# Performance work log

Measured on AMD Instinct MI355X. Metric: run time of the kernel, lower is better.

## Reference

```python
import jax, jax.numpy as jnp
import numpy as np

B, M = 64, 2048
D_LLM = 4096
D_T, D_P, D_C = 256, 512, 1024
NH_T, NH_P, NH_C = 4, 8, 16
S_T, S_P, S_C = 4, 8, 4
LN_EPS = 1e-5


def setup_inputs() -> dict:
    key = jax.random.key(0)
    ks = iter(jax.random.split(key, 48))
    def n(shape, s=0.02):
        return jax.random.normal(next(ks), shape, jnp.float32) * s
    inp = {
        "hidden_state": jax.random.normal(next(ks), (B, D_LLM), jnp.float32),
        "time_fiber": jax.random.normal(next(ks), (M, D_T), jnp.float32),
        "topic_fiber": jax.random.normal(next(ks), (M, D_P), jnp.float32),
        "ctx_fiber": jax.random.normal(next(ks), (M, D_C), jnp.float32),
        "mem_mask": jnp.zeros((B, M), bool),
        # BundleQueryHeads: Linear(d_LLM -> d_F_*) per bundle (torch weight layout (out,in))
        "Wq_time": n((D_T, D_LLM)), "bq_time": jnp.zeros((D_T,), jnp.float32),
        "Wq_topic": n((D_P, D_LLM)), "bq_topic": jnp.zeros((D_P,), jnp.float32),
        "Wq_ctx": n((D_C, D_LLM)), "bq_ctx": jnp.zeros((D_C,), jnp.float32),
        # nn.MultiheadAttention packed in_proj (3d, d) and out_proj (d, d)
        "Wqkv_time": n((3 * D_T, D_T)), "bqkv_time": jnp.zeros((3 * D_T,), jnp.float32),
        "Wo_time": n((D_T, D_T)), "bo_time": jnp.zeros((D_T,), jnp.float32),
        "Wqkv_topic": n((3 * D_P, D_P)), "bqkv_topic": jnp.zeros((3 * D_P,), jnp.float32),
        "Wo_topic": n((D_P, D_P)), "bo_topic": jnp.zeros((D_P,), jnp.float32),
        "Wqkv_ctx": n((3 * D_C, D_C)), "bqkv_ctx": jnp.zeros((3 * D_C,), jnp.float32),
        "Wo_ctx": n((D_C, D_C)), "bo_ctx": jnp.zeros((D_C,), jnp.float32),
        # per-slot lifts stacked: (slots, d_F, d_LLM) for einsum 'bd,sde->bse'
        "Wlift_time": n((S_T, D_T, D_LLM)), "blift_time": jnp.zeros((S_T, D_LLM), jnp.float32),
        "Wlift_topic": n((S_P, D_P, D_LLM)), "blift_topic": jnp.zeros((S_P, D_LLM), jnp.float32),
        "Wlift_ctx": n((S_C, D_C, D_LLM)), "blift_ctx": jnp.zeros((S_C, D_LLM), jnp.float32),
        "ln_g": jnp.ones((D_LLM,), jnp.float32),
        "ln_b": jnp.zeros((D_LLM,), jnp.float32),
    }
    return inp


def _mha1(q, kv, Wqkv, bqkv, Wo, bo, nh, mask):
    """Single-query-token MHA. q: (B,d); kv: (M,d) shared across batch; mask: (B,M) True=ignore."""
    d = q.shape[-1]
    hd = d // nh
    Wq, Wk, Wv = jnp.split(Wqkv, 3, axis=0)
    bq, bk, bv = jnp.split(bqkv, 3, axis=0)
    qp = (q @ Wq.T + bq).reshape(-1, nh, hd)    # (B,h,hd)
    kp = (kv @ Wk.T + bk).reshape(-1, nh, hd)   # (M,h,hd)
    vp = (kv @ Wv.T + bv).reshape(-1, nh, hd)   # (M,h,hd)
    scale = 1.0 / np.float32(np.sqrt(hd))
    scores = jnp.einsum('bhd,mhd->bhm', qp, kp) * scale  # (B,h,M)
    scores = jnp.where(mask[:, None, :], jnp.float32(-1e9), scores)
    attn = jax.nn.softmax(scores, axis=-1)
    out = jnp.einsum('bhm,mhd->bhd', attn, vp).reshape(-1, d)  # (B,d)
    return out @ Wo.T + bo


def _layernorm(x, g, b):
    mu = jnp.mean(x, axis=-1, keepdims=True)
    var = jnp.mean((x - mu) ** 2, axis=-1, keepdims=True)
    return (x - mu) * jax.lax.rsqrt(var + LN_EPS) * g + b


def reference(hidden_state, time_fiber, topic_fiber, ctx_fiber, mem_mask,
              Wq_time, bq_time, Wq_topic, bq_topic, Wq_ctx, bq_ctx,
              Wqkv_time, bqkv_time, Wo_time, bo_time,
              Wqkv_topic, bqkv_topic, Wo_topic, bo_topic,
              Wqkv_ctx, bqkv_ctx, Wo_ctx, bo_ctx,
              Wlift_time, blift_time, Wlift_topic, blift_topic, Wlift_ctx, blift_ctx,
              ln_g, ln_b):
    # bundle query heads
    q_time = hidden_state @ Wq_time.T + bq_time
    q_topic = hidden_state @ Wq_topic.T + bq_topic
    q_ctx = hidden_state @ Wq_ctx.T + bq_ctx
    # three single-token cross attentions
    o_time = _mha1(q_time, time_fiber, Wqkv_time, bqkv_time, Wo_time, bo_time, NH_T, mem_mask)
    o_topic = _mha1(q_topic, topic_fiber, Wqkv_topic, bqkv_topic, Wo_topic, bo_topic, NH_P, mem_mask)
    o_ctx = _mha1(q_ctx, ctx_fiber, Wqkv_ctx, bqkv_ctx, Wo_ctx, bo_ctx, NH_C, mem_mask)
    # per-slot lifts, batched across slots
    slots_time = jnp.einsum('bd,sde->bse', o_time, Wlift_time) + blift_time[None]
    slots_topic = jnp.einsum('bd,sde->bse', o_topic, Wlift_topic) + blift_topic[None]
    slots_ctx = jnp.einsum('bd,sde->bse', o_ctx, Wlift_ctx) + blift_ctx[None]
    prefix = jnp.concatenate([slots_time, slots_topic, slots_ctx], axis=1)  # (B, L_mem, d_LLM)
    return _layernorm(prefix, ln_g, ln_b)
```

## Files before the change

kernel.cpp:

```cpp
#include <hip/hip_runtime.h>
#include <cstdint>
#include <cstddef>

typedef __attribute__((ext_vector_type(8))) short short8;
typedef __attribute__((ext_vector_type(4))) float floatx4;

__device__ __forceinline__ unsigned short f2bf(float f) {
    unsigned int u = __builtin_bit_cast(unsigned int, f);
    u += 0x7fffu + ((u >> 16) & 1u);
    return (unsigned short)(u >> 16);
}
__device__ __forceinline__ float bflo(unsigned int u) {
    return __builtin_bit_cast(float, u << 16);
}
__device__ __forceinline__ short8 pack8(float4 a, float4 b) {
    short8 r;
    r[0] = (short)f2bf(a.x); r[1] = (short)f2bf(a.y);
    r[2] = (short)f2bf(a.z); r[3] = (short)f2bf(a.w);
    r[4] = (short)f2bf(b.x); r[5] = (short)f2bf(b.y);
    r[6] = (short)f2bf(b.z); r[7] = (short)f2bf(b.w);
    return r;
}

struct SubGemm {
    const float* A; const float* W; const float* bias;
    float* Cf; unsigned short* Ch;
    int K, N, Kc, nj, ni, nkz, mode, ldc;
};
struct GemmBatch { SubGemm d[16]; int start[16]; int nd; };

__global__ __launch_bounds__(256) void gemm_batch(GemmBatch gb)
{
    __shared__ short As[64 * 40];
    __shared__ __align__(16) char Braw[32 * 132 * 4];
    short* Bs  = (short*)Braw;
    float* Bsf = (float*)Braw;

    const int bx = blockIdx.x;
    int di = 0;
#pragma unroll 1
    for (int i = 1; i < gb.nd; ++i) if (bx >= gb.start[i]) di = i;
    const SubGemm g = gb.d[di];
    int local = bx - gb.start[di];
    const int jb = local % g.nj; local /= g.nj;
    const int ib = local % g.ni;
    const int kz = local / g.ni;

    const int tid = threadIdx.x;
    const int w = tid >> 6, lane = tid & 63;
    const int quad = lane >> 4, l16 = lane & 15;
    const int noff = w * 32;

    const int rA = tid >> 2, cA = (tid & 3) * 8;
    const float* pa = g.A + (size_t)(ib * 64 + rA) * g.K + kz * g.Kc + cA;

    floatx4 acc[4][2] = {};

    if (g.mode <= 1) {
        const int rB = tid >> 1, cB = (tid & 1) * 16;
        const float* pb = g.W + (size_t)(jb * 128 + rB) * g.K + kz * g.Kc + cB;
        float4 a0 = *(const float4*)(pa), a1 = *(const float4*)(pa + 4);
        float4 b0 = *(const float4*)(pb),     b1 = *(const float4*)(pb + 4);
        float4 b2 = *(const float4*)(pb + 8), b3 = *(const float4*)(pb + 12);
#pragma unroll 1
        for (int k0 = 0; k0 < g.Kc; k0 += 32) {
            *(short8*)&As[rA * 40 + cA]     = pack8(a0, a1);
            *(short8*)&Bs[rB * 40 + cB]     = pack8(b0, b1);
            *(short8*)&Bs[rB * 40 + cB + 8] = pack8(b2, b3);
            __syncthreads();
            if (k0 + 32 < g.Kc) {
                pa += 32; pb += 32;
                a0 = *(const float4*)(pa);     a1 = *(const float4*)(pa + 4);
                b0 = *(const float4*)(pb);     b1 = *(const float4*)(pb + 4);
                b2 = *(const float4*)(pb + 8); b3 = *(const float4*)(pb + 12);
            }
            short8 af[4], bfr[2];
#pragma unroll
            for (int r = 0; r < 4; ++r)
                af[r] = *(const short8*)&As[(r * 16 + l16) * 40 + quad * 8];
#pragma unroll
            for (int c = 0; c < 2; ++c)
                bfr[c] = *(const short8*)&Bs[(noff + c * 16 + l16) * 40 + quad * 8];
#pragma unroll
            for (int r = 0; r < 4; ++r)
#pragma unroll
                for (int c = 0; c < 2; ++c)
                    acc[r][c] = __builtin_amdgcn_mfma_f32_16x16x32_bf16(af[r], bfr[c], acc[r][c], 0, 0, 0);
            __syncthreads();
        }
    } else {
        const int rK = tid >> 3, cN = (tid & 7) * 16;
        const float* pb = g.W + (size_t)rK * g.N + jb * 128 + cN;
        float4 a0 = *(const float4*)(pa), a1 = *(const float4*)(pa + 4);
        float4 b0 = *(const float4*)(pb),     b1 = *(const float4*)(pb + 4);
        float4 b2 = *(const float4*)(pb + 8), b3 = *(const float4*)(pb + 12);
#pragma unroll 1
        for (int k0 = 0; k0 < g.Kc; k0 += 32) {
            *(short8*)&As[rA * 40 + cA] = pack8(a0, a1);
            *(float4*)&Bsf[rK * 132 + cN]      = b0;
            *(float4*)&Bsf[rK * 132 + cN + 4]  = b1;
            *(float4*)&Bsf[rK * 132 + cN + 8]  = b2;
            *(float4*)&Bsf[rK * 132 + cN + 12] = b3;
            __syncthreads();
            if (k0 + 32 < g.Kc) {
                pa += 32; pb += (size_t)32 * g.N;
                a0 = *(const float4*)(pa);     a1 = *(const float4*)(pa + 4);
                b0 = *(const float4*)(pb);     b1 = *(const float4*)(pb + 4);
                b2 = *(const float4*)(pb + 8); b3 = *(const float4*)(pb + 12);
            }
            short8 af[4], bfr[2];
#pragma unroll
            for (int r = 0; r < 4; ++r)
                af[r] = *(const short8*)&As[(r * 16 + l16) * 40 + quad * 8];
#pragma unroll
            for (int c = 0; c < 2; ++c) {
                const int colb = noff + c * 16 + l16;
#pragma unroll
                for (int i = 0; i < 8; ++i)
                    bfr[c][i] = (short)f2bf(Bsf[(quad * 8 + i) * 132 + colb]);
            }
#pragma unroll
            for (int r = 0; r < 4; ++r)
#pragma unroll
                for (int c = 0; c < 2; ++c)
                    acc[r][c] = __builtin_amdgcn_mfma_f32_16x16x32_bf16(af[r], bfr[c], acc[r][c], 0, 0, 0);
            __syncthreads();
        }
    }

#pragma unroll
    for (int r = 0; r < 4; ++r)
#pragma unroll
        for (int c = 0; c < 2; ++c) {
            const int col = jb * 128 + noff + c * 16 + l16;
            const float bj = (g.mode == 1 && kz != 0) ? 0.f : g.bias[col];
#pragma unroll
            for (int q = 0; q < 4; ++q) {
                const int row = ib * 64 + r * 16 + quad * 4 + q;
                const float v = acc[r][c][q] + bj;
                if (g.mode == 0)
                    g.Ch[(size_t)row * g.ldc + col] = f2bf(v);
                else if (g.mode == 1) {
                    if (g.nkz > 1) atomicAdd(&g.Cf[(size_t)row * g.ldc + col], v);
                    else           g.Cf[(size_t)row * g.ldc + col] = v;
                } else
                    g.Cf[(size_t)row * g.ldc + col] = v;
            }
        }
}

__global__ __launch_bounds__(256) void qk_batch(
    const float* __restrict__ qp_t, const float* __restrict__ qp_p, const float* __restrict__ qp_c,
    const unsigned short* __restrict__ kv_t, const unsigned short* __restrict__ kv_p, const unsigned short* __restrict__ kv_c,
    float* __restrict__ S_t, float* __restrict__ S_p, float* __restrict__ S_c)
{
    __shared__ short As[64 * 72];
    __shared__ short Bs[128 * 72];
    const int hy = blockIdx.y;
    const float* qp; const unsigned short* kv; float* S; int d, h;
    if (hy < 4)       { qp = qp_t; kv = kv_t; S = S_t; d = 256;  h = hy; }
    else if (hy < 12) { qp = qp_p; kv = kv_p; S = S_p; d = 512;  h = hy - 4; }
    else              { qp = qp_c; kv = kv_c; S = S_c; d = 1024; h = hy - 12; }

    const int j0 = blockIdx.x * 128;
    const int tid = threadIdx.x;
    const int w = tid >> 6, lane = tid & 63;
    const int quad = lane >> 4, l16 = lane & 15;
    const int noff = w * 32;
    const int twoD = 2 * d;

    {
        const int b = tid >> 2, kc = (tid & 3) * 16;
        const float* ga = qp + (size_t)b * d + h * 64 + kc;
        float4 a0 = *(const float4*)(ga + 0), a1 = *(const float4*)(ga + 4);
        float4 a2 = *(const float4*)(ga + 8), a3 = *(const float4*)(ga + 12);
        *(short8*)&As[b * 72 + kc + 0] = pack8(a0, a1);
        *(short8*)&As[b * 72 + kc + 8] = pack8(a2, a3);
    }
    {
        const int m = tid >> 1, hf = (tid & 1) * 32;
        const unsigned short* gb = kv + (size_t)(j0 + m) * twoD + h * 64 + hf;
        uint4 b0 = *(const uint4*)(gb + 0),  b1 = *(const uint4*)(gb + 8);
        uint4 b2 = *(const uint4*)(gb + 16), b3 = *(const uint4*)(gb + 24);
        *(uint4*)&Bs[m * 72 + hf + 0]  = b0;
        *(uint4*)&Bs[m * 72 + hf + 8]  = b1;
        *(uint4*)&Bs[m * 72 + hf + 16] = b2;
        *(uint4*)&Bs[m * 72 + hf + 24] = b3;
    }
    __syncthreads();

    floatx4 acc[4][2] = {};
#pragma unroll
    for (int k0 = 0; k0 < 64; k0 += 32) {
        short8 af[4], bfr[2];
#pragma unroll
        for (int r = 0; r < 4; ++r)
            af[r] = *(const short8*)&As[(r * 16 + l16) * 72 + k0 + quad * 8];
#pragma unroll
        for (int c = 0; c < 2; ++c)
            bfr[c] = *(const short8*)&Bs[(noff + c * 16 + l16) * 72 + k0 + quad * 8];
#pragma unroll
        for (int r = 0; r < 4; ++r)
#pragma unroll
            for (int c = 0; c < 2; ++c)
                acc[r][c] = __builtin_amdgcn_mfma_f32_16x16x32_bf16(af[r], bfr[c], acc[r][c], 0, 0, 0);
    }
#pragma unroll
    for (int r = 0; r < 4; ++r)
#pragma unroll
        for (int c = 0; c < 2; ++c) {
            int col = j0 + noff + c * 16 + l16;
#pragma unroll
            for (int q = 0; q < 4; ++q) {
                int row = r * 16 + quad * 4 + q;
                S[((size_t)h * 64 + row) * 2048 + col] = acc[r][c][q] * 0.125f;
            }
        }
}

__global__ __launch_bounds__(256) void softmax_pv_batch(
    const float* __restrict__ S_t, const float* __restrict__ S_p, const float* __restrict__ S_c,
    const unsigned short* __restrict__ kv_t, const unsigned short* __restrict__ kv_p, const unsigned short* __restrict__ kv_c,
    const uint8_t* __restrict__ mask,
    float* __restrict__ o_t, float* __restrict__ o_p, float* __restrict__ o_c)
{
    const int hy = blockIdx.x, b = blockIdx.y;
    const float* S; const unsigned short* kv; float* o; int d, h;
    if (hy < 4)       { S = S_t; kv = kv_t; o = o_t; d = 256;  h = hy; }
    else if (hy < 12) { S = S_p; kv = kv_p; o = o_p; d = 512;  h = hy - 4; }
    else              { S = S_c; kv = kv_c; o = o_c; d = 1024; h = hy - 12; }

    const int tid = threadIdx.x;
    __shared__ __align__(16) float sc[2048];
    __shared__ float red[4];
    __shared__ float part[4][64];
    __shared__ float s_max, s_sum;

    const float* Sr = S + ((size_t)h * 64 + b) * 2048;
    const uint8_t* mr = mask + (size_t)b * 2048;

    float lmax = -1e30f;
    for (int m = tid; m < 2048; m += 256) {
        float s = Sr[m];
        if (mr[m]) s = -1e9f;
        sc[m] = s;
        lmax = fmaxf(lmax, s);
    }
#pragma unroll
    for (int off = 32; off; off >>= 1) lmax = fmaxf(lmax, __shfl_down(lmax, off));
    if ((tid & 63) == 0) red[tid >> 6] = lmax;
    __syncthreads();
    if (tid == 0) s_max = fmaxf(fmaxf(red[0], red[1]), fmaxf(red[2], red[3]));
    __syncthreads();
    const float mx = s_max;

    float lsum = 0.f;
    for (int m = tid; m < 2048; m += 256) {
        float e = __expf(sc[m] - mx);
        sc[m] = e;
        lsum += e;
    }
#pragma unroll
    for (int off = 32; off; off >>= 1) lsum += __shfl_down(lsum, off);
    if ((tid & 63) == 0) red[tid >> 6] = lsum;
    __syncthreads();
    if (tid == 0) s_sum = red[0] + red[1] + red[2] + red[3];
    __syncthreads();

    const int lane = tid & 63, w = tid >> 6;
    const int twoD = 2 * d;
    const unsigned short* vcol = kv + d + h * 64 + lane;
    float acc = 0.f;
    const int m0 = w * 512;
#pragma unroll 1
    for (int m = m0; m < m0 + 512; m += 8) {
#pragma unroll
        for (int j = 0; j < 8; ++j)
            acc += sc[m + j] * bflo((unsigned int)vcol[(size_t)(m + j) * twoD]);
    }
    part[w][lane] = acc;
    __syncthreads();
    if (tid < 64) {
        float r = (part[0][tid] + part[1][tid] + part[2][tid] + part[3][tid]) / s_sum;
        o[(size_t)b * d + h * 64 + tid] = r;
    }
}

__global__ __launch_bounds__(256) void ln_kernel(
    float* __restrict__ x, const float* __restrict__ g, const float* __restrict__ bb)
{
    const int row = blockIdx.x;
    float* xr = x + (size_t)row * 4096;
    const int tid = threadIdx.x;
    float v[16];
    float sum = 0.f, sumsq = 0.f;
#pragma unroll
    for (int i = 0; i < 16; ++i) {
        v[i] = xr[tid + i * 256];
        sum += v[i];
        sumsq += v[i] * v[i];
    }
    __shared__ float rs[4], rq[4];
#pragma unroll
    for (int off = 32; off; off >>= 1) {
        sum += __shfl_down(sum, off);
        sumsq += __shfl_down(sumsq, off);
    }
    if ((tid & 63) == 0) { rs[tid >> 6] = sum; rq[tid >> 6] = sumsq; }
    __syncthreads();
    const float ts = rs[0] + rs[1] + rs[2] + rs[3];
    const float tq = rq[0] + rq[1] + rq[2] + rq[3];
    const float mu = ts * (1.f / 4096.f);
    const float var = tq * (1.f / 4096.f) - mu * mu;
    const float r = rsqrtf(var + 1e-5f);
#pragma unroll
    for (int i = 0; i < 16; ++i) {
        int e = tid + i * 256;
        xr[e] = (v[i] - mu) * r * g[e] + bb[e];
    }
}

static void addg(GemmBatch& G, int& tot,
                 const float* A, const float* W, const float* bias,
                 float* Cf, unsigned short* Ch,
                 int K, int N, int Kc, int nj, int ni, int nkz, int mode, int ldc)
{
    SubGemm& s = G.d[G.nd];
    s.A = A; s.W = W; s.bias = bias; s.Cf = Cf; s.Ch = Ch;
    s.K = K; s.N = N; s.Kc = Kc; s.nj = nj; s.ni = ni; s.nkz = nkz;
    s.mode = mode; s.ldc = ldc;
    G.start[G.nd] = tot;
    tot += nj * ni * nkz;
    G.nd++;
}

extern "C" void kernel_launch(void* const* d_in, const int* in_sizes, int n_in,
                              void* d_out, int out_size, void* d_ws, size_t ws_size,
                              hipStream_t stream)
{
    const float*   hs     = (const float*)d_in[0];
    const float*   fib_t  = (const float*)d_in[1];
    const float*   fib_p  = (const float*)d_in[2];
    const float*   fib_c  = (const float*)d_in[3];
    const uint8_t* mask   = (const uint8_t*)d_in[4];
    const float* Wq_t   = (const float*)d_in[5];  const float* bq_t   = (const float*)d_in[6];
    const float* Wq_p   = (const float*)d_in[7];  const float* bq_p   = (const float*)d_in[8];
    const float* Wq_c   = (const float*)d_in[9];  const float* bq_c   = (const float*)d_in[10];
    const float* Wqkv_t = (const float*)d_in[11]; const float* bqkv_t = (const float*)d_in[12];
    const float* Wo_t   = (const float*)d_in[13]; const float* bo_t   = (const float*)d_in[14];
    const float* Wqkv_p = (const float*)d_in[15]; const float* bqkv_p = (const float*)d_in[16];
    const float* Wo_p   = (const float*)d_in[17]; const float* bo_p   = (const float*)d_in[18];
    const float* Wqkv_c = (const float*)d_in[19]; const float* bqkv_c = (const float*)d_in[20];
    const float* Wo_c   = (const float*)d_in[21]; const float* bo_c   = (const float*)d_in[22];
    const float* Wl_t   = (const float*)d_in[23]; const float* bl_t   = (const float*)d_in[24];
    const float* Wl_p   = (const float*)d_in[25]; const float* bl_p   = (const float*)d_in[26];
    const float* Wl_c   = (const float*)d_in[27]; const float* bl_c   = (const float*)d_in[28];
    const float* ln_g   = (const float*)d_in[29]; const float* ln_b   = (const float*)d_in[30];

    char* wsb = (char*)d_ws;
    float* q_t  = (float*)wsb; wsb += 64 * 256 * 4;
    float* q_p  = (float*)wsb; wsb += 64 * 512 * 4;
    float* q_c  = (float*)wsb; wsb += 64 * 1024 * 4;
    float* qp_t = (float*)wsb; wsb += 64 * 256 * 4;
    float* qp_p = (float*)wsb; wsb += 64 * 512 * 4;
    float* qp_c = (float*)wsb; wsb += 64 * 1024 * 4;
    float* po_t = (float*)wsb; wsb += 64 * 256 * 4;
    float* po_p = (float*)wsb; wsb += 64 * 512 * 4;
    float* po_c = (float*)wsb; wsb += 64 * 1024 * 4;
    size_t zbytes = (size_t)(wsb - (char*)d_ws);
    float* o_t  = (float*)wsb; wsb += 64 * 256 * 4;
    float* o_p  = (float*)wsb; wsb += 64 * 512 * 4;
    float* o_c  = (float*)wsb; wsb += 64 * 1024 * 4;
    unsigned short* kv_t = (unsigned short*)wsb; wsb += 2048 * 512 * 2;
    unsigned short* kv_p = (unsigned short*)wsb; wsb += 2048 * 1024 * 2;
    unsigned short* kv_c = (unsigned short*)wsb; wsb += 2048 * 2048 * 2;
    float* S_t = (float*)wsb; wsb += (size_t)4  * 64 * 2048 * 4;
    float* S_p = (float*)wsb; wsb += (size_t)8  * 64 * 2048 * 4;
    float* S_c = (float*)wsb; wsb += (size_t)16 * 64 * 2048 * 4;
    float* out = (float*)d_out;

    const dim3 blk(256);
    hipMemsetAsync(d_ws, 0, zbytes, stream);

    {
        GemmBatch G{}; int tot = 0; G.nd = 0;
        addg(G, tot, fib_c, Wqkv_c + 1024 * 1024, bqkv_c + 1024, nullptr, kv_c, 1024, 2048, 1024, 16, 32, 1, 0, 2048);
        addg(G, tot, fib_p, Wqkv_p + 512 * 512,   bqkv_p + 512,  nullptr, kv_p, 512,  1024, 512,  8,  32, 1, 0, 1024);
        addg(G, tot, fib_t, Wqkv_t + 256 * 256,   bqkv_t + 256,  nullptr, kv_t, 256,  512,  256,  4,  32, 1, 0, 512);
        addg(G, tot, hs, Wq_c, bq_c, q_c, nullptr, 4096, 1024, 256, 8, 1, 16, 1, 1024);
        addg(G, tot, hs, Wq_p, bq_p, q_p, nullptr, 4096, 512,  256, 4, 1, 16, 1, 512);
        addg(G, tot, hs, Wq_t, bq_t, q_t, nullptr, 4096, 256,  256, 2, 1, 16, 1, 256);
        gemm_batch<<<dim3(tot), blk, 0, stream>>>(G);
    }

    {
        GemmBatch G{}; int tot = 0; G.nd = 0;
        addg(G, tot, q_c, Wqkv_c, bqkv_c, qp_c, nullptr, 1024, 1024, 128, 8, 1, 8, 1, 1024);
        addg(G, tot, q_p, Wqkv_p, bqkv_p, qp_p, nullptr, 512,  512,  64,  4, 1, 8, 1, 512);
        addg(G, tot, q_t, Wqkv_t, bqkv_t, qp_t, nullptr, 256,  256,  64,  2, 1, 4, 1, 256);
        gemm_batch<<<dim3(tot), blk, 0, stream>>>(G);
    }

    qk_batch<<<dim3(16, 28), blk, 0, stream>>>(qp_t, qp_p, qp_c, kv_t, kv_p, kv_c, S_t, S_p, S_c);
    softmax_pv_batch<<<dim3(28, 64), blk, 0, stream>>>(S_t, S_p, S_c, kv_t, kv_p, kv_c, mask, o_t, o_p, o_c);

    {
        GemmBatch G{}; int tot = 0; G.nd = 0;
        addg(G, tot, o_c, Wo_c, bo_c, po_c, nullptr, 1024, 1024, 128, 8, 1, 8, 1, 1024);
        addg(G, tot, o_p, Wo_p, bo_p, po_p, nullptr, 512,  512,  64,  4, 1, 8, 1, 512);
        addg(G, tot, o_t, Wo_t, bo_t, po_t, nullptr, 256,  256,  64,  2, 1, 4, 1, 256);
        gemm_batch<<<dim3(tot), blk, 0, stream>>>(G);
    }

    {
        GemmBatch G{}; int tot = 0; G.nd = 0;
        for (int z = 0; z < 4; ++z)
            addg(G, tot, po_c, Wl_c + (size_t)z * 1024 * 4096, bl_c + z * 4096,
                 out + (size_t)(12 + z) * 4096, nullptr, 1024, 4096, 1024, 32, 1, 1, 2, 16 * 4096);
        for (int z = 0; z < 8; ++z)
            addg(G, tot, po_p, Wl_p + (size_t)z * 512 * 4096, bl_p + z * 4096,
                 out + (size_t)(4 + z) * 4096, nullptr, 512, 4096, 512, 32, 1, 1, 2, 16 * 4096);
        for (int z = 0; z < 4; ++z)
            addg(G, tot, po_t, Wl_t + (size_t)z * 256 * 4096, bl_t + z * 4096,
                 out + (size_t)z * 4096, nullptr, 256, 4096, 256, 32, 1, 1, 2, 16 * 4096);
        gemm_batch<<<dim3(tot), blk, 0, stream>>>(G);
    }

    ln_kernel<<<dim3(1024), blk, 0, stream>>>(out, ln_g, ln_b);
}
```

Baseline: 393.6 us.

## Double-buffer GEMM LDS tiles, split-K lift GEMMs, fold lift bias into layernorm

```diff
diff --git a/kernel.cpp b/kernel.cpp
--- a/kernel.cpp
+++ b/kernel.cpp
@@ -31,10 +31,8 @@
 
 __global__ __launch_bounds__(256) void gemm_batch(GemmBatch gb)
 {
-    __shared__ short As[64 * 40];
-    __shared__ __align__(16) char Braw[32 * 132 * 4];
-    short* Bs  = (short*)Braw;
-    float* Bsf = (float*)Braw;
+    __shared__ short As[2][64 * 40];
+    __shared__ __align__(16) char Braw[2][32 * 132 * 4];
 
     const int bx = blockIdx.x;
     int di = 0;
@@ -62,69 +60,108 @@
         float4 a0 = *(const float4*)(pa), a1 = *(const float4*)(pa + 4);
         float4 b0 = *(const float4*)(pb),     b1 = *(const float4*)(pb + 4);
         float4 b2 = *(const float4*)(pb + 8), b3 = *(const float4*)(pb + 12);
+        {
+            short* Asp = As[0]; short* Bsp = (short*)Braw[0];
+            *(short8*)&Asp[rA * 40 + cA]     = pack8(a0, a1);
+            *(short8*)&Bsp[rB * 40 + cB]     = pack8(b0, b1);
+            *(short8*)&Bsp[rB * 40 + cB + 8] = pack8(b2, b3);
+        }
+        if (g.Kc > 32) {
+            pa += 32; pb += 32;
+            a0 = *(const float4*)(pa);     a1 = *(const float4*)(pa + 4);
+            b0 = *(const float4*)(pb);     b1 = *(const float4*)(pb + 4);
+            b2 = *(const float4*)(pb + 8); b3 = *(const float4*)(pb + 12);
+        }
+        int cur = 0;
 #pragma unroll 1
         for (int k0 = 0; k0 < g.Kc; k0 += 32) {
-            *(short8*)&As[rA * 40 + cA]     = pack8(a0, a1);
-            *(short8*)&Bs[rB * 40 + cB]     = pack8(b0, b1);
-            *(short8*)&Bs[rB * 40 + cB + 8] = pack8(b2, b3);
             __syncthreads();
-            if (k0 + 32 < g.Kc) {
-                pa += 32; pb += 32;
-                a0 = *(const float4*)(pa);     a1 = *(const float4*)(pa + 4);
-                b0 = *(const float4*)(pb);     b1 = *(const float4*)(pb + 4);
-                b2 = *(const float4*)(pb + 8); b3 = *(const float4*)(pb + 12);
-            }
+            const short* Asc = As[cur];
+            const short* Bsc = (const short*)Braw[cur];
             short8 af[4], bfr[2];
 #pragma unroll
             for (int r = 0; r < 4; ++r)
-                af[r] = *(const short8*)&As[(r * 16 + l16) * 40 + quad * 8];
+                af[r] = *(const short8*)&Asc[(r * 16 + l16) * 40 + quad * 8];
 #pragma unroll
             for (int c = 0; c < 2; ++c)
-                bfr[c] = *(const short8*)&Bs[(noff + c * 16 + l16) * 40 + quad * 8];
+                bfr[c] = *(const short8*)&Bsc[(noff + c * 16 + l16) * 40 + quad * 8];
 #pragma unroll
             for (int r = 0; r < 4; ++r)
 #pragma unroll
                 for (int c = 0; c < 2; ++c)
                     acc[r][c] = __builtin_amdgcn_mfma_f32_16x16x32_bf16(af[r], bfr[c], acc[r][c], 0, 0, 0);
-            __syncthreads();
+            if (k0 + 32 < g.Kc) {
+                short* Asn = As[cur ^ 1]; short* Bsn = (short*)Braw[cur ^ 1];
+                *(short8*)&Asn[rA * 40 + cA]     = pack8(a0, a1);
+                *(short8*)&Bsn[rB * 40 + cB]     = pack8(b0, b1);
+                *(short8*)&Bsn[rB * 40 + cB + 8] = pack8(b2, b3);
+                if (k0 + 64 < g.Kc) {
+                    pa += 32; pb += 32;
+                    a0 = *(const float4*)(pa);     a1 = *(const float4*)(pa + 4);
+                    b0 = *(const float4*)(pb);     b1 = *(const float4*)(pb + 4);
+                    b2 = *(const float4*)(pb + 8); b3 = *(const float4*)(pb + 12);
+                }
+            }
+            cur ^= 1;
         }
     } else {
         const int rK = tid >> 3, cN = (tid & 7) * 16;
-        const float* pb = g.W + (size_t)rK * g.N + jb * 128 + cN;
+        const int cNs = cN ^ ((rK & 8) << 1);
+        const float* pb = g.W + (size_t)(kz * g.Kc + rK) * g.N + jb * 128 + cN;
         float4 a0 = *(const float4*)(pa), a1 = *(const float4*)(pa + 4);
         float4 b0 = *(const float4*)(pb),     b1 = *(const float4*)(pb + 4);
         float4 b2 = *(const float4*)(pb + 8), b3 = *(const float4*)(pb + 12);
+        {
+            short* Asp = As[0]; float* Bp = (float*)Braw[0];
+            *(short8*)&Asp[rA * 40 + cA] = pack8(a0, a1);
+            *(float4*)&Bp[rK * 132 + cNs]      = b0;
+            *(float4*)&Bp[rK * 132 + cNs + 4]  = b1;
+            *(float4*)&Bp[rK * 132 + cNs + 8]  = b2;
+            *(float4*)&Bp[rK * 132 + cNs + 12] = b3;
+        }
+        if (g.Kc > 32) {
+            pa += 32; pb += (size_t)32 * g.N;
+            a0 = *(const float4*)(pa);     a1 = *(const float4*)(pa + 4);
+            b0 = *(const float4*)(pb);     b1 = *(const float4*)(pb + 4);
+            b2 = *(const float4*)(pb + 8); b3 = *(const float4*)(pb + 12);
+        }
+        int cur = 0;
 #pragma unroll 1
         for (int k0 = 0; k0 < g.Kc; k0 += 32) {
-            *(short8*)&As[rA * 40 + cA] = pack8(a0, a1);
-            *(float4*)&Bsf[rK * 132 + cN]      = b0;
-            *(float4*)&Bsf[rK * 132 + cN + 4]  = b1;
-            *(float4*)&Bsf[rK * 132 + cN + 8]  = b2;
-            *(float4*)&Bsf[rK * 132 + cN + 12] = b3;
             __syncthreads();
-            if (k0 + 32 < g.Kc) {
-                pa += 32; pb += (size_t)32 * g.N;
-                a0 = *(const float4*)(pa);     a1 = *(const float4*)(pa + 4);
-                b0 = *(const float4*)(pb);     b1 = *(const float4*)(pb + 4);
-                b2 = *(const float4*)(pb + 8); b3 = *(const float4*)(pb + 12);
-            }
+            const short* Asc = As[cur];
+            const float* Bc = (const float*)Braw[cur];
             short8 af[4], bfr[2];
 #pragma unroll
             for (int r = 0; r < 4; ++r)
-                af[r] = *(const short8*)&As[(r * 16 + l16) * 40 + quad * 8];
+                af[r] = *(const short8*)&Asc[(r * 16 + l16) * 40 + quad * 8];
 #pragma unroll
             for (int c = 0; c < 2; ++c) {
-                const int colb = noff + c * 16 + l16;
+                const int colb = (noff + c * 16 + l16) ^ ((quad & 1) << 4);
 #pragma unroll
                 for (int i = 0; i < 8; ++i)
-                    bfr[c][i] = (short)f2bf(Bsf[(quad * 8 + i) * 132 + colb]);
+                    bfr[c][i] = (short)f2bf(Bc[(quad * 8 + i) * 132 + colb]);
             }
 #pragma unroll
             for (int r = 0; r < 4; ++r)
 #pragma unroll
                 for (int c = 0; c < 2; ++c)
                     acc[r][c] = __builtin_amdgcn_mfma_f32_16x16x32_bf16(af[r], bfr[c], acc[r][c], 0, 0, 0);
-            __syncthreads();
+            if (k0 + 32 < g.Kc) {
+                short* Asn = As[cur ^ 1]; float* Bn = (float*)Braw[cur ^ 1];
+                *(short8*)&Asn[rA * 40 + cA] = pack8(a0, a1);
+                *(float4*)&Bn[rK * 132 + cNs]      = b0;
+                *(float4*)&Bn[rK * 132 + cNs + 4]  = b1;
+                *(float4*)&Bn[rK * 132 + cNs + 8]  = b2;
+                *(float4*)&Bn[rK * 132 + cNs + 12] = b3;
+                if (k0 + 64 < g.Kc) {
+                    pa += 32; pb += (size_t)32 * g.N;
+                    a0 = *(const float4*)(pa);     a1 = *(const float4*)(pa + 4);
+                    b0 = *(const float4*)(pb);     b1 = *(const float4*)(pb + 4);
+                    b2 = *(const float4*)(pb + 8); b3 = *(const float4*)(pb + 12);
+                }
+            }
+            cur ^= 1;
         }
     }
 
@@ -133,7 +170,8 @@
 #pragma unroll
         for (int c = 0; c < 2; ++c) {
             const int col = jb * 128 + noff + c * 16 + l16;
-            const float bj = (g.mode == 1 && kz != 0) ? 0.f : g.bias[col];
+            const float bj = (g.bias == nullptr) ? 0.f
+                           : ((g.mode == 1 && kz != 0) ? 0.f : g.bias[col]);
 #pragma unroll
             for (int q = 0; q < 4; ++q) {
                 const int row = ib * 64 + r * 16 + quad * 4 + q;
@@ -143,8 +181,10 @@
                 else if (g.mode == 1) {
                     if (g.nkz > 1) atomicAdd(&g.Cf[(size_t)row * g.ldc + col], v);
                     else           g.Cf[(size_t)row * g.ldc + col] = v;
-                } else
-                    g.Cf[(size_t)row * g.ldc + col] = v;
+                } else {
+                    if (g.nkz > 1) atomicAdd(&g.Cf[(size_t)row * g.ldc + col], v);
+                    else           g.Cf[(size_t)row * g.ldc + col] = v;
+                }
             }
         }
 }
@@ -287,16 +327,22 @@
 }
 
 __global__ __launch_bounds__(256) void ln_kernel(
-    float* __restrict__ x, const float* __restrict__ g, const float* __restrict__ bb)
+    float* __restrict__ x, const float* __restrict__ g, const float* __restrict__ bb,
+    const float* __restrict__ blt, const float* __restrict__ blp, const float* __restrict__ blc)
 {
     const int row = blockIdx.x;
+    const int l = row & 15;
+    const float* lb = (l < 4)  ? (blt + (size_t)l * 4096)
+                    : (l < 12) ? (blp + (size_t)(l - 4) * 4096)
+                               : (blc + (size_t)(l - 12) * 4096);
     float* xr = x + (size_t)row * 4096;
     const int tid = threadIdx.x;
     float v[16];
     float sum = 0.f, sumsq = 0.f;
 #pragma unroll
     for (int i = 0; i < 16; ++i) {
-        v[i] = xr[tid + i * 256];
+        int e = tid + i * 256;
+        v[i] = xr[e] + lb[e];
         sum += v[i];
         sumsq += v[i] * v[i];
     }
@@ -381,6 +427,7 @@
 
     const dim3 blk(256);
     hipMemsetAsync(d_ws, 0, zbytes, stream);
+    hipMemsetAsync(d_out, 0, (size_t)out_size, stream);
 
     {
         GemmBatch G{}; int tot = 0; G.nd = 0;
@@ -415,16 +462,16 @@
     {
         GemmBatch G{}; int tot = 0; G.nd = 0;
         for (int z = 0; z < 4; ++z)
-            addg(G, tot, po_c, Wl_c + (size_t)z * 1024 * 4096, bl_c + z * 4096,
-                 out + (size_t)(12 + z) * 4096, nullptr, 1024, 4096, 1024, 32, 1, 1, 2, 16 * 4096);
+            addg(G, tot, po_c, Wl_c + (size_t)z * 1024 * 4096, nullptr,
+                 out + (size_t)(12 + z) * 4096, nullptr, 1024, 4096, 256, 32, 1, 4, 2, 16 * 4096);
         for (int z = 0; z < 8; ++z)
-            addg(G, tot, po_p, Wl_p + (size_t)z * 512 * 4096, bl_p + z * 4096,
-                 out + (size_t)(4 + z) * 4096, nullptr, 512, 4096, 512, 32, 1, 1, 2, 16 * 4096);
+            addg(G, tot, po_p, Wl_p + (size_t)z * 512 * 4096, nullptr,
+                 out + (size_t)(4 + z) * 4096, nullptr, 512, 4096, 256, 32, 1, 2, 2, 16 * 4096);
         for (int z = 0; z < 4; ++z)
-            addg(G, tot, po_t, Wl_t + (size_t)z * 256 * 4096, bl_t + z * 4096,
+            addg(G, tot, po_t, Wl_t + (size_t)z * 256 * 4096, nullptr,
                  out + (size_t)z * 4096, nullptr, 256, 4096, 256, 32, 1, 1, 2, 16 * 4096);
         gemm_batch<<<dim3(tot), blk, 0, stream>>>(G);
     }
 
-    ln_kernel<<<dim3(1024), blk, 0, stream>>>(out, ln_g, ln_b);
-}
+    ln_kernel<<<dim3(1024), blk, 0, stream>>>(out, ln_g, ln_b, bl_t, bl_p, bl_c);
+}
```

After: 402.0 us. 1.02x slower.
